# Kernel optimization log

Measured on AMD Instinct MI355X. Metric: run time of the kernel, lower is better.

## Reference

```python
import jax, jax.numpy as jnp
import numpy as np

D_MODEL = 1024
D_PROJ = D_MODEL // 4


def setup_inputs() -> dict:
    key = jax.random.key(0)
    k1, k2, k3 = jax.random.split(key, 3)
    hidden_states = jax.random.normal(k1, (4, 2048, D_MODEL), dtype=jnp.float32)
    proj_w = jax.random.normal(k2, (D_PROJ, D_MODEL), dtype=jnp.float32) * 0.02
    proj_b = jnp.zeros((D_PROJ,), dtype=jnp.float32)
    clf_w = jax.random.normal(k3, (1, 1), dtype=jnp.float32) * 0.02
    clf_b = jnp.zeros((1,), dtype=jnp.float32)
    return {"hidden_states": hidden_states, "proj_w": proj_w, "proj_b": proj_b,
            "clf_w": clf_w, "clf_b": clf_b}


def reference(hidden_states, proj_w, proj_b, clf_w, clf_b):
    # h: [B, S, D/4]
    h = jax.nn.relu(jnp.einsum('bsd,pd->bsp', hidden_states, proj_w) + proj_b)
    # pairwise dot products == batched h @ h^T: [B, S, S]
    scores = jnp.einsum('bip,bjp->bij', h, h)
    # scalar affine classifier (Linear(1,1)) folded in
    return scores * clf_w[0, 0] + clf_b[0]
```

## Files before the change

### kernel.cpp

```cpp
#include <hip/hip_runtime.h>
#include <hip/hip_bf16.h>

typedef __bf16 bf16_t;
typedef __attribute__((ext_vector_type(8))) __bf16 bf16x8;
typedef __attribute__((ext_vector_type(4))) float f32x4;

#define SEQ    2048
#define DMODEL 1024
#define DPROJ  256
#define NBATCH 4

__device__ __forceinline__ bf16x8 cvt8(const float4& lo, const float4& hi) {
    bf16x8 v;
    v[0] = (bf16_t)lo.x; v[1] = (bf16_t)lo.y; v[2] = (bf16_t)lo.z; v[3] = (bf16_t)lo.w;
    v[4] = (bf16_t)hi.x; v[5] = (bf16_t)hi.y; v[6] = (bf16_t)hi.z; v[7] = (bf16_t)hi.w;
    return v;
}

__device__ __forceinline__ void gl_lds16(const void* g, void* l) {
    __builtin_amdgcn_global_load_lds(
        (const __attribute__((address_space(1))) unsigned int*)g,
        (__attribute__((address_space(3))) unsigned int*)l, 16, 0, 0);
}

__global__ __launch_bounds__(256, 2) void proj_kernel(
    const float* __restrict__ X, const float* __restrict__ W,
    const float* __restrict__ bias, bf16_t* __restrict__ H)
{
    __shared__ __align__(16) bf16_t Xs[2][64 * 64];
    __shared__ __align__(16) bf16_t Ws[2][64 * 64];

    const int m0 = blockIdx.x * 64;
    const int n0 = blockIdx.y * 64;
    const int tid  = threadIdx.x;
    const int lane = tid & 63;
    const int wave = tid >> 6;
    const int quad = lane >> 4;
    const int l16  = lane & 15;
    const int wm = (wave & 1) * 32;
    const int wn = (wave >> 1) * 32;
    const int swz = l16 & 7;

    int srow[2], scol[2], soff[2];
    #pragma unroll
    for (int r = 0; r < 2; ++r) {
        const int p = r * 256 + tid;
        srow[r] = p >> 3;
        scol[r] = p & 7;
        soff[r] = srow[r] * 64 + ((scol[r] ^ (srow[r] & 7)) * 8);
    }

    float4 xr[2][2][2], wr[2][2][2];

    #pragma unroll
    for (int s = 0; s < 2; ++s) {
        const int k0 = s * 64;
        #pragma unroll
        for (int r = 0; r < 2; ++r) {
            const float* gx = X + (size_t)(m0 + srow[r]) * DMODEL + k0 + scol[r] * 8;
            xr[s][r][0] = *(const float4*)gx;
            xr[s][r][1] = *(const float4*)(gx + 4);
            const float* gw = W + (size_t)(n0 + srow[r]) * DMODEL + k0 + scol[r] * 8;
            wr[s][r][0] = *(const float4*)gw;
            wr[s][r][1] = *(const float4*)(gw + 4);
        }
    }

    f32x4 acc[2][2] = {};

    #pragma unroll
    for (int kt = 0; kt < 16; ++kt) {
        const int s = kt & 1;

        #pragma unroll
        for (int r = 0; r < 2; ++r) {
            *(bf16x8*)&Xs[s][soff[r]] = cvt8(xr[s][r][0], xr[s][r][1]);
            *(bf16x8*)&Ws[s][soff[r]] = cvt8(wr[s][r][0], wr[s][r][1]);
        }
        __syncthreads();

        if (kt < 14) {
            const int k0 = (kt + 2) * 64;
            #pragma unroll
            for (int r = 0; r < 2; ++r) {
                const float* gx = X + (size_t)(m0 + srow[r]) * DMODEL + k0 + scol[r] * 8;
                xr[s][r][0] = *(const float4*)gx;
                xr[s][r][1] = *(const float4*)(gx + 4);
                const float* gw = W + (size_t)(n0 + srow[r]) * DMODEL + k0 + scol[r] * 8;
                wr[s][r][0] = *(const float4*)gw;
                wr[s][r][1] = *(const float4*)(gw + 4);
            }
        }

        #pragma unroll
        for (int ks = 0; ks < 2; ++ks) {
            bf16x8 af[2], bfr[2];
            #pragma unroll
            for (int i = 0; i < 2; ++i) {
                const int ch = (((ks << 2) | quad) ^ swz) * 8;
                af[i]  = *(const bf16x8*)&Xs[s][(wm + i * 16 + l16) * 64 + ch];
                bfr[i] = *(const bf16x8*)&Ws[s][(wn + i * 16 + l16) * 64 + ch];
            }
            #pragma unroll
            for (int i = 0; i < 2; ++i)
                #pragma unroll
                for (int j = 0; j < 2; ++j)
                    acc[i][j] = __builtin_amdgcn_mfma_f32_16x16x32_bf16(
                        af[i], bfr[j], acc[i][j], 0, 0, 0);
        }
    }

    #pragma unroll
    for (int i = 0; i < 2; ++i) {
        #pragma unroll
        for (int j = 0; j < 2; ++j) {
            const int gn = n0 + wn + j * 16 + l16;
            const float bv = bias[gn];
            #pragma unroll
            for (int r = 0; r < 4; ++r) {
                const int gm = m0 + wm + i * 16 + quad * 4 + r;
                float v = acc[i][j][r] + bv;
                v = v > 0.f ? v : 0.f;
                H[(size_t)gm * DPROJ + gn] = (bf16_t)v;
            }
        }
    }
}

__global__ __launch_bounds__(256, 8) void score_kernel(
    const bf16_t* __restrict__ H, const float* __restrict__ clf_w,
    const float* __restrict__ clf_b, float* __restrict__ Out)
{
    __shared__ __align__(16) bf16_t As[64 * 64];
    __shared__ __align__(16) bf16_t Bs[64 * 64];

    int t = blockIdx.x, bi = 0, rl = SEQ / 64;
    while (t >= rl) { t -= rl; --rl; ++bi; }
    const int bj = bi + t;
    const int b  = blockIdx.y;
    const int m0 = bi * 64;
    const int n0 = bj * 64;
    const bf16_t* Hb = H + (size_t)b * SEQ * DPROJ;
    float* Ob = Out + (size_t)b * SEQ * SEQ;

    const int tid  = threadIdx.x;
    const int lane = tid & 63;
    const int wave = tid >> 6;
    const int quad = lane >> 4;
    const int l16  = lane & 15;
    const int wm = (wave & 1) * 32;
    const int wn = (wave >> 1) * 32;
    const int swz = l16 & 7;

    const bf16_t* gA[2];
    const bf16_t* gB[2];
    bf16_t* lA[2];
    bf16_t* lB[2];
    #pragma unroll
    for (int t2 = 0; t2 < 2; ++t2) {
        const int g   = (wave * 2 + t2) * 64 + lane;
        const int row = g >> 3;
        const int gc  = (g & 7) ^ (row & 7);
        gA[t2] = Hb + (size_t)(m0 + row) * DPROJ + gc * 8;
        gB[t2] = Hb + (size_t)(n0 + row) * DPROJ + gc * 8;
        lA[t2] = As + (wave * 2 + t2) * 512;
        lB[t2] = Bs + (wave * 2 + t2) * 512;
    }

    f32x4 acc[2][2] = {};

    for (int kt = 0; kt < 4; ++kt) {
        __syncthreads();
        #pragma unroll
        for (int t2 = 0; t2 < 2; ++t2) {
            gl_lds16(gA[t2], lA[t2]);
            gl_lds16(gB[t2], lB[t2]);
        }
        __syncthreads();
        #pragma unroll
        for (int t2 = 0; t2 < 2; ++t2) { gA[t2] += 64; gB[t2] += 64; }

        #pragma unroll
        for (int ks = 0; ks < 2; ++ks) {
            const int ch = (((ks << 2) | quad) ^ swz) * 8;
            bf16x8 af[2], bfr[2];
            #pragma unroll
            for (int i = 0; i < 2; ++i) {
                af[i]  = *(const bf16x8*)&As[(wm + i * 16 + l16) * 64 + ch];
                bfr[i] = *(const bf16x8*)&Bs[(wn + i * 16 + l16) * 64 + ch];
            }
            #pragma unroll
            for (int i = 0; i < 2; ++i)
                #pragma unroll
                for (int j = 0; j < 2; ++j)
                    acc[i][j] = __builtin_amdgcn_mfma_f32_16x16x32_bf16(
                        af[i], bfr[j], acc[i][j], 0, 0, 0);
        }
    }

    const float scale = clf_w[0];
    const float off   = clf_b[0];

    #pragma unroll
    for (int i = 0; i < 2; ++i)
        #pragma unroll
        for (int j = 0; j < 2; ++j)
            #pragma unroll
            for (int r = 0; r < 4; ++r) {
                const int gm = m0 + wm + i * 16 + quad * 4 + r;
                const int gn = n0 + wn + j * 16 + l16;
                Ob[(size_t)gm * SEQ + gn] = acc[i][j][r] * scale + off;
            }

    if (bi != bj) {
        #pragma unroll
        for (int i = 0; i < 2; ++i)
            #pragma unroll
            for (int j = 0; j < 2; ++j) {
                const int gn = n0 + wn + j * 16 + l16;
                const int gm = m0 + wm + i * 16 + quad * 4;
                float4 v;
                v.x = acc[i][j][0] * scale + off;
                v.y = acc[i][j][1] * scale + off;
                v.z = acc[i][j][2] * scale + off;
                v.w = acc[i][j][3] * scale + off;
                *(float4*)&Ob[(size_t)gn * SEQ + gm] = v;
            }
    }
}

extern "C" void kernel_launch(void* const* d_in, const int* in_sizes, int n_in,
                              void* d_out, int out_size, void* d_ws, size_t ws_size,
                              hipStream_t stream) {
    const float* X    = (const float*)d_in[0];
    const float* W    = (const float*)d_in[1];
    const float* bias = (const float*)d_in[2];
    const float* clfw = (const float*)d_in[3];
    const float* clfb = (const float*)d_in[4];
    float* Out = (float*)d_out;
    bf16_t* H  = (bf16_t*)d_ws;

    dim3 g1(NBATCH * SEQ / 64, DPROJ / 64, 1);
    proj_kernel<<<g1, 256, 0, stream>>>(X, W, bias, H);

    const int ntile = SEQ / 64;
    dim3 g2(ntile * (ntile + 1) / 2, NBATCH);
    score_kernel<<<g2, 256, 0, stream>>>(H, clfw, clfb, Out);
}
```

Baseline: 122.1 us.

## Retile projection GEMM to 32x256 blocks so X is read once

```diff
diff --git a/kernel.cpp b/kernel.cpp
--- a/kernel.cpp
+++ b/kernel.cpp
@@ -23,70 +23,71 @@
         (__attribute__((address_space(3))) unsigned int*)l, 16, 0, 0);
 }
 
-__global__ __launch_bounds__(256, 2) void proj_kernel(
+__global__ __launch_bounds__(256, 1) void proj_kernel(
     const float* __restrict__ X, const float* __restrict__ W,
     const float* __restrict__ bias, bf16_t* __restrict__ H)
 {
-    __shared__ __align__(16) bf16_t Xs[2][64 * 64];
-    __shared__ __align__(16) bf16_t Ws[2][64 * 64];
-
-    const int m0 = blockIdx.x * 64;
-    const int n0 = blockIdx.y * 64;
+    __shared__ __align__(16) bf16_t Xs[2][32 * 64];
+    __shared__ __align__(16) bf16_t Ws[2][256 * 64];
+
+    const int m0 = blockIdx.x * 32;
     const int tid  = threadIdx.x;
     const int lane = tid & 63;
     const int wave = tid >> 6;
     const int quad = lane >> 4;
     const int l16  = lane & 15;
-    const int wm = (wave & 1) * 32;
-    const int wn = (wave >> 1) * 32;
-    const int swz = l16 & 7;
-
-    int srow[2], scol[2], soff[2];
-    #pragma unroll
-    for (int r = 0; r < 2; ++r) {
+    const int wn   = wave * 64;
+    const int swz  = l16 & 7;
+
+    const int xrow = tid >> 3;
+    const int xcol = tid & 7;
+    const int xoff = xrow * 64 + ((xcol ^ (xrow & 7)) * 8);
+    int wrow[8], wcol[8], woff[8];
+    #pragma unroll
+    for (int r = 0; r < 8; ++r) {
         const int p = r * 256 + tid;
-        srow[r] = p >> 3;
-        scol[r] = p & 7;
-        soff[r] = srow[r] * 64 + ((scol[r] ^ (srow[r] & 7)) * 8);
-    }
-
-    float4 xr[2][2][2], wr[2][2][2];
+        wrow[r] = p >> 3;
+        wcol[r] = p & 7;
+        woff[r] = wrow[r] * 64 + ((wcol[r] ^ (wrow[r] & 7)) * 8);
+    }
+
+    float4 xr[2][2];
+    float4 wr[2][8][2];
 
     #pragma unroll
     for (int s = 0; s < 2; ++s) {
         const int k0 = s * 64;
-        #pragma unroll
-        for (int r = 0; r < 2; ++r) {
-            const float* gx = X + (size_t)(m0 + srow[r]) * DMODEL + k0 + scol[r] * 8;
-            xr[s][r][0] = *(const float4*)gx;
-            xr[s][r][1] = *(const float4*)(gx + 4);
-            const float* gw = W + (size_t)(n0 + srow[r]) * DMODEL + k0 + scol[r] * 8;
+        const float* gx = X + (size_t)(m0 + xrow) * DMODEL + k0 + xcol * 8;
+        xr[s][0] = *(const float4*)gx;
+        xr[s][1] = *(const float4*)(gx + 4);
+        #pragma unroll
+        for (int r = 0; r < 8; ++r) {
+            const float* gw = W + (size_t)wrow[r] * DMODEL + k0 + wcol[r] * 8;
             wr[s][r][0] = *(const float4*)gw;
             wr[s][r][1] = *(const float4*)(gw + 4);
         }
     }
 
-    f32x4 acc[2][2] = {};
+    f32x4 acc[2][4] = {};
 
     #pragma unroll
     for (int kt = 0; kt < 16; ++kt) {
         const int s = kt & 1;
 
-        #pragma unroll
-        for (int r = 0; r < 2; ++r) {
-            *(bf16x8*)&Xs[s][soff[r]] = cvt8(xr[s][r][0], xr[s][r][1]);
-            *(bf16x8*)&Ws[s][soff[r]] = cvt8(wr[s][r][0], wr[s][r][1]);
-        }
+        *(bf16x8*)&Xs[s][xoff] = cvt8(xr[s][0], xr[s][1]);
+        #pragma unroll
+        for (int r = 0; r < 8; ++r)
+            *(bf16x8*)&Ws[s][woff[r]] = cvt8(wr[s][r][0], wr[s][r][1]);
         __syncthreads();
 
         if (kt < 14) {
             const int k0 = (kt + 2) * 64;
-            #pragma unroll
-            for (int r = 0; r < 2; ++r) {
-                const float* gx = X + (size_t)(m0 + srow[r]) * DMODEL + k0 + scol[r] * 8;
-                xr[s][r][0] = *(const float4*)gx;
-                xr[s][r][1] = *(const float4*)(gx + 4);
-                const float* gw = W + (size_t)(n0 + srow[r]) * DMODEL + k0 + scol[r] * 8;
+            const float* gx = X + (size_t)(m0 + xrow) * DMODEL + k0 + xcol * 8;
+            xr[s][0] = *(const float4*)gx;
+            xr[s][1] = *(const float4*)(gx + 4);
+            #pragma unroll
+            for (int r = 0; r < 8; ++r) {
+                const float* gw = W + (size_t)wrow[r] * DMODEL + k0 + wcol[r] * 8;
                 wr[s][r][0] = *(const float4*)gw;
                 wr[s][r][1] = *(const float4*)(gw + 4);
             }
@@ -94,17 +95,18 @@
 
         #pragma unroll
         for (int ks = 0; ks < 2; ++ks) {
-            bf16x8 af[2], bfr[2];
-            #pragma unroll
-            for (int i = 0; i < 2; ++i) {
-                const int ch = (((ks << 2) | quad) ^ swz) * 8;
-                af[i]  = *(const bf16x8*)&Xs[s][(wm + i * 16 + l16) * 64 + ch];
-                bfr[i] = *(const bf16x8*)&Ws[s][(wn + i * 16 + l16) * 64 + ch];
-            }
+            const int ch = (((ks << 2) | quad) ^ swz) * 8;
+            bf16x8 af[2], bfr[4];
+            #pragma unroll
+            for (int i = 0; i < 2; ++i)
+                af[i] = *(const bf16x8*)&Xs[s][(i * 16 + l16) * 64 + ch];
+            #pragma unroll
+            for (int j = 0; j < 4; ++j)
+                bfr[j] = *(const bf16x8*)&Ws[s][(wn + j * 16 + l16) * 64 + ch];
             #pragma unroll
             for (int i = 0; i < 2; ++i)
                 #pragma unroll
-                for (int j = 0; j < 2; ++j)
+                for (int j = 0; j < 4; ++j)
                     acc[i][j] = __builtin_amdgcn_mfma_f32_16x16x32_bf16(
                         af[i], bfr[j], acc[i][j], 0, 0, 0);
         }
@@ -113,12 +115,12 @@
     #pragma unroll
     for (int i = 0; i < 2; ++i) {
         #pragma unroll
-        for (int j = 0; j < 2; ++j) {
-            const int gn = n0 + wn + j * 16 + l16;
+        for (int j = 0; j < 4; ++j) {
+            const int gn = wn + j * 16 + l16;
             const float bv = bias[gn];
             #pragma unroll
             for (int r = 0; r < 4; ++r) {
-                const int gm = m0 + wm + i * 16 + quad * 4 + r;
+                const int gm = m0 + i * 16 + quad * 4 + r;
                 float v = acc[i][j][r] + bv;
                 v = v > 0.f ? v : 0.f;
                 H[(size_t)gm * DPROJ + gn] = (bf16_t)v;
@@ -240,7 +242,7 @@
     float* Out = (float*)d_out;
     bf16_t* H  = (bf16_t*)d_ws;
 
-    dim3 g1(NBATCH * SEQ / 64, DPROJ / 64, 1);
+    dim3 g1(NBATCH * SEQ / 32, 1, 1);
     proj_kernel<<<g1, 256, 0, stream>>>(X, W, bias, H);
 
     const int ntile = SEQ / 64;
```

Measured after the change: 124.0 us. Within noise of the previous version (+1.6%).
